# Kernel tuning notes

Hardware: AMD Instinct MI355X
Metric: run time of the kernel (lower is better)

Reference implementation:

```python
import jax, jax.numpy as jnp
import numpy as np

B, T, K = 32, 8192, 16
EPS = 1e-7
LAM_FIRE, LAM_CANCEL, LAM_VALID, LAM_WRITE = 1.0, 1.0, 0.5, 0.5


def setup_inputs() -> dict:
    key = jax.random.key(0)
    ks = jax.random.split(key, 11)
    return {
        "trigger_hazard": jax.random.uniform(ks[0], (B, T, K), jnp.float32),
        "validity": jax.random.uniform(ks[1], (B, T, K), jnp.float32),
        "cancel_logits": jax.random.normal(ks[2], (B, T, K, 3), jnp.float32),
        "write_score": jax.random.normal(ks[3], (B, T, 1), jnp.float32),
        "live_mask": jax.random.randint(ks[4], (B, T, K), 0, 2).astype(bool),
        "contract_id": jax.random.randint(ks[5], (B, T, K), 0, 32),
        "oracle_fire": jax.random.randint(ks[6], (B, T, K), 0, 2).astype(jnp.float32),
        "oracle_cancel": jax.random.randint(ks[7], (B, T, K), 0, 4),
        "oracle_valid": jax.random.randint(ks[8], (B, T, K), 0, 2).astype(jnp.float32),
        "oracle_should_write": jax.random.randint(ks[9], (B, T, 1), 0, 2).astype(jnp.float32),
        "oracle_contract_id": jax.random.randint(ks[10], (B, T, K), 0, 32),
    }


def _masked_bce(p_raw, y, m):
    # Mirrors torch: BCE(clamp(p)*mask, y*mask), then *mask, sum / clamp(mask.sum(),1)
    n = jnp.maximum(m.sum(), 1.0)
    p = jnp.clip(p_raw, EPS, 1.0 - EPS) * m
    t = y * m
    # extra inner clip only guards masked entries (p==0), which are zeroed anyway
    bce = -(t * jnp.log(jnp.clip(p, EPS)) + (1.0 - t) * jnp.log(jnp.clip(1.0 - p, EPS)))
    return (bce * m).sum() / n


def _cancel_ce(logits, cancel_tgt, live_mask):
    has = ((cancel_tgt > 0) & live_mask).astype(jnp.float32)  # (B,T,K)
    n = has.sum()
    tgt = jnp.clip(cancel_tgt - 1, 0).astype(jnp.int32)
    logp = jax.nn.log_softmax(logits, axis=-1)  # (B,T,K,3)
    ce = -jnp.take_along_axis(logp, tgt[..., None], axis=-1)[..., 0]
    return jnp.where(n > 0, (ce * has).sum() / jnp.maximum(n, 1.0), 0.0)


def _bce_with_logits(x, y):
    return jnp.mean(jnp.maximum(x, 0.0) - x * y + jnp.log1p(jnp.exp(-jnp.abs(x))))


def reference(trigger_hazard, validity, cancel_logits, write_score, live_mask,
              contract_id, oracle_fire, oracle_cancel, oracle_valid,
              oracle_should_write, oracle_contract_id):
    # Vectorized align_oracle_to_model: broadcast compare + first-match argmax + gather
    match = (contract_id[..., :, None] == oracle_contract_id[..., None, :]) \
            & (contract_id != 0)[..., None]              # (B,T,Km,Ko)
    found = match.any(axis=-1)                           # (B,T,Km)
    idx = jnp.argmax(match, axis=-1)                     # first matching oracle slot

    def align_f(x):  # float tensors -> zeros where unmatched (torch out = zeros float)
        return jnp.where(found, jnp.take_along_axis(x, idx, axis=2), 0.0)

    fire_t = align_f(oracle_fire)
    valid_t = align_f(oracle_valid)
    cancel_t = jnp.where(found, jnp.take_along_axis(oracle_cancel, idx, axis=2), 0)

    m = live_mask.astype(jnp.float32)
    fire = LAM_FIRE * _masked_bce(trigger_hazard, fire_t, m)
    cancel = LAM_CANCEL * _cancel_ce(cancel_logits, cancel_t, live_mask)
    valid = LAM_VALID * _masked_bce(validity, valid_t, m)
    write = LAM_WRITE * _bce_with_logits(write_score, oracle_should_write)
    total = fire + cancel + valid + write
    return jnp.stack([fire, cancel, valid, write, total])
```

## Files before the change

### kernel.cpp

```cpp
#include <hip/hip_runtime.h>
#include <math.h>

#define EPS_F 1e-7f

constexpr int Bc = 32, Tc = 8192, Kc = 16;
constexpr int ROWS  = Bc * Tc;
constexpr int BLOCK = 256;
constexpr int ROWS_PER_BLK = BLOCK / 4;
constexpr int NBLK  = ROWS / ROWS_PER_BLK;

typedef unsigned long long u64;

__device__ __forceinline__ u64 shflx64(u64 v, int m) {
  unsigned lo = __shfl_xor((unsigned)v, m, 64);
  unsigned hi = __shfl_xor((unsigned)(v >> 32), m, 64);
  return ((u64)hi << 32) | lo;
}

__global__ __launch_bounds__(BLOCK) void loss_main(
    const float* __restrict__ trig,
    const float* __restrict__ valp,
    const float* __restrict__ clog,
    const float* __restrict__ wscore,
    const int*   __restrict__ live,
    const int*   __restrict__ cid,
    const float* __restrict__ ofire,
    const int*   __restrict__ ocan,
    const float* __restrict__ ovalid,
    const float* __restrict__ oshw,
    const int*   __restrict__ ocid,
    float* __restrict__ part)
{
  const int t    = blockIdx.x * BLOCK + threadIdx.x;
  const int lane = threadIdx.x & 63;

  const int4   oc = ((const int4*)  ocid)[t];
  const int4   cc = ((const int4*)  ocan)[t];
  const float4 ff = ((const float4*)ofire)[t];
  const float4 vv = ((const float4*)ovalid)[t];
  const int4   cd = ((const int4*)  cid)[t];
  const int4   lm = ((const int4*)  live)[t];
  const float4 ph = ((const float4*)trig)[t];
  const float4 pq = ((const float4*)valp)[t];
  const float4 lA = ((const float4*)clog)[t * 3 + 0];
  const float4 lB = ((const float4*)clog)[t * 3 + 1];
  const float4 lC = ((const float4*)clog)[t * 3 + 2];
  float ws_x = 0.f, ws_y = 0.f;
  if (threadIdx.x < ROWS_PER_BLK) {
    const int r2 = blockIdx.x * ROWS_PER_BLK + threadIdx.x;
    ws_x = wscore[r2];
    ws_y = oshw[r2];
  }

  u64 tblLo = 0ull, tblHi = 0ull, fndLo = 0ull, fndHi = 0ull;
  {
    const int   ocs[4] = {oc.x, oc.y, oc.z, oc.w};
    const int   ccs[4] = {cc.x, cc.y, cc.z, cc.w};
    const float ffs[4] = {ff.x, ff.y, ff.z, ff.w};
    const float vvs[4] = {vv.x, vv.y, vv.z, vv.w};
    #pragma unroll
    for (int j = 0; j < 4; ++j) {
      const unsigned c  = (unsigned)ocs[j] & 31u;
      const unsigned sh = (c & 15u) * 4u;
      const bool isLo   = c < 16u;
      const u64 fsel    = isLo ? fndLo : fndHi;
      const bool seen   = ((fsel >> sh) & 1ull) != 0ull;
      const unsigned nib = (unsigned)ffs[j] | ((unsigned)vvs[j] << 1) |
                           ((unsigned)ccs[j] << 2);
      const u64 add  = seen ? 0ull : ((u64)nib << sh);
      const u64 fadd = 0xFull << sh;
      tblLo |= isLo ? add : 0ull;
      tblHi |= isLo ? 0ull : add;
      fndLo |= isLo ? fadd : 0ull;
      fndHi |= isLo ? 0ull : fadd;
    }
  }

  #pragma unroll
  for (int m = 1; m <= 2; m <<= 1) {
    const u64 pTL = shflx64(tblLo, m);
    const u64 pTH = shflx64(tblHi, m);
    const u64 pFL = shflx64(fndLo, m);
    const u64 pFH = shflx64(fndHi, m);
    const bool iLow = (lane & m) == 0;
    const u64 loTL = iLow ? tblLo : pTL, hiTL = iLow ? pTL : tblLo;
    const u64 loTH = iLow ? tblHi : pTH, hiTH = iLow ? pTH : tblHi;
    const u64 loFL = iLow ? fndLo : pFL, hiFL = iLow ? pFL : fndLo;
    const u64 loFH = iLow ? fndHi : pFH, hiFH = iLow ? pFH : fndHi;
    tblLo = loTL | (hiTL & ~loFL);
    tblHi = loTH | (hiTH & ~loFH);
    fndLo = loFL | hiFL;
    fndHi = loFH | hiFH;
  }

  float s0 = 0.f, s1 = 0.f, s2 = 0.f, s3 = 0.f, s4 = 0.f;
  {
    const int   cds[4] = {cd.x, cd.y, cd.z, cd.w};
    const int   lms[4] = {lm.x, lm.y, lm.z, lm.w};
    const float phs[4] = {ph.x, ph.y, ph.z, ph.w};
    const float pqs[4] = {pq.x, pq.y, pq.z, pq.w};
    const float L0[4] = {lA.x, lA.w, lB.z, lC.y};
    const float L1[4] = {lA.y, lB.x, lB.w, lC.z};
    const float L2[4] = {lA.z, lB.y, lC.x, lC.w};
    #pragma unroll
    for (int j = 0; j < 4; ++j) {
      const unsigned c  = (unsigned)cds[j] & 31u;
      const unsigned sh = (c & 15u) * 4u;
      const bool isLo   = c < 16u;
      const bool fnd = (c != 0u) &&
                       ((((isLo ? fndLo : fndHi) >> sh) & 1ull) != 0ull);
      unsigned nib = (unsigned)(((isLo ? tblLo : tblHi) >> sh)) & 15u;
      nib = fnd ? nib : 0u;
      const float fire_t = (float)(nib & 1u);
      const float val_t  = (float)((nib >> 1) & 1u);
      const int   can_t  = (int)(nib >> 2);

      const float m = lms[j] ? 1.f : 0.f;

      const float p  = fminf(fmaxf(phs[j], EPS_F), 1.f - EPS_F);
      const float bf = -__logf((fire_t != 0.f) ? p : 1.f - p);
      const float q  = fminf(fmaxf(pqs[j], EPS_F), 1.f - EPS_F);
      const float bv = -__logf((val_t != 0.f) ? q : 1.f - q);

      const float has = (can_t > 0 && lms[j]) ? 1.f : 0.f;
      const int tgt = (can_t - 1) < 0 ? 0 : (can_t - 1);
      const float l0 = L0[j], l1 = L1[j], l2 = L2[j];
      const float mx  = fmaxf(l0, fmaxf(l1, l2));
      const float lse = mx + __logf(__expf(l0 - mx) + __expf(l1 - mx) +
                                    __expf(l2 - mx));
      const float lt  = (tgt == 0) ? l0 : ((tgt == 1) ? l1 : l2);

      s0 += bf * m;
      s1 += m;
      s2 += (lse - lt) * has;
      s3 += has;
      s4 += bv * m;
    }
  }

  float s5 = 0.f;
  if (threadIdx.x < ROWS_PER_BLK) {
    s5 = fmaxf(ws_x, 0.f) - ws_x * ws_y + __logf(1.f + __expf(-fabsf(ws_x)));
  }

  float v[6] = {s0, s1, s2, s3, s4, s5};
  #pragma unroll
  for (int off = 32; off > 0; off >>= 1) {
    #pragma unroll
    for (int i = 0; i < 6; ++i) v[i] += __shfl_down(v[i], off, 64);
  }
  __shared__ float red[4][6];
  const int w = threadIdx.x >> 6;
  if (lane == 0) {
    #pragma unroll
    for (int i = 0; i < 6; ++i) red[w][i] = v[i];
  }
  __syncthreads();
  if (threadIdx.x == 0) {
    #pragma unroll
    for (int i = 0; i < 6; ++i)
      part[blockIdx.x * 6 + i] = red[0][i] + red[1][i] + red[2][i] + red[3][i];
  }
}

__global__ __launch_bounds__(BLOCK) void loss_finalize(
    const float* __restrict__ part, float* __restrict__ out)
{
  double v[6] = {0, 0, 0, 0, 0, 0};
  for (int r = threadIdx.x; r < NBLK; r += BLOCK) {
    #pragma unroll
    for (int i = 0; i < 6; ++i) v[i] += (double)part[r * 6 + i];
  }
  #pragma unroll
  for (int off = 32; off > 0; off >>= 1) {
    #pragma unroll
    for (int i = 0; i < 6; ++i) v[i] += __shfl_down(v[i], off, 64);
  }
  __shared__ double red[4][6];
  const int w = threadIdx.x >> 6, lane = threadIdx.x & 63;
  if (lane == 0) {
    #pragma unroll
    for (int i = 0; i < 6; ++i) red[w][i] = v[i];
  }
  __syncthreads();
  if (threadIdx.x == 0) {
    double a[6];
    #pragma unroll
    for (int i = 0; i < 6; ++i) a[i] = red[0][i] + red[1][i] + red[2][i] + red[3][i];
    const double live_n = a[1] < 1.0 ? 1.0 : a[1];
    const double fire   = a[0] / live_n;
    const double cancel = (a[3] > 0.0) ? a[2] / (a[3] < 1.0 ? 1.0 : a[3])
                                       : 0.0;
    const double valid  = 0.5 * a[4] / live_n;
    const double wr     = 0.5 * a[5] / (double)ROWS;
    out[0] = (float)fire;
    out[1] = (float)cancel;
    out[2] = (float)valid;
    out[3] = (float)wr;
    out[4] = (float)(fire + cancel + valid + wr);
  }
}

extern "C" void kernel_launch(void* const* d_in, const int* in_sizes, int n_in,
                              void* d_out, int out_size, void* d_ws, size_t ws_size,
                              hipStream_t stream) {
  const float* trig   = (const float*)d_in[0];
  const float* valp   = (const float*)d_in[1];
  const float* clog   = (const float*)d_in[2];
  const float* wscore = (const float*)d_in[3];
  const int*   live   = (const int*)  d_in[4];
  const int*   cid    = (const int*)  d_in[5];
  const float* ofire  = (const float*)d_in[6];
  const int*   ocan   = (const int*)  d_in[7];
  const float* ovalid = (const float*)d_in[8];
  const float* oshw   = (const float*)d_in[9];
  const int*   ocid   = (const int*)  d_in[10];
  float* out  = (float*)d_out;
  float* part = (float*)d_ws;

  loss_main<<<NBLK, BLOCK, 0, stream>>>(trig, valp, clog, wscore, live, cid,
                                        ofire, ocan, ovalid, oshw, ocid, part);
  loss_finalize<<<1, BLOCK, 0, stream>>>(part, out);
}
```

Before: 214.2 us.

## Use persistent-style blocks with double-buffered register prefetch of the next row group

Shrinks the grid from one row-group per thread to 1024 blocks that each loop over four strided items, prefetching the next item's loads into a second register buffer while the current one is computed. It also moves the write-score load to every fourth thread and sets a launch bound of two blocks per unit. The aim is to overlap memory latency with compute and cut the number of partial sums the finalize kernel has to reduce. In exchange, the doubled register buffers raise register pressure and lower the number of waves available to hide latency.

Result: no change. 213.1 us (-0.5%).

```diff
diff --git a/kernel.cpp b/kernel.cpp
--- a/kernel.cpp
+++ b/kernel.cpp
@@ -4,10 +4,11 @@
 #define EPS_F 1e-7f
 
 constexpr int Bc = 32, Tc = 8192, Kc = 16;
-constexpr int ROWS  = Bc * Tc;
-constexpr int BLOCK = 256;
-constexpr int ROWS_PER_BLK = BLOCK / 4;
-constexpr int NBLK  = ROWS / ROWS_PER_BLK;
+constexpr int ROWS   = Bc * Tc;
+constexpr int BLOCK  = 256;
+constexpr int NBLK   = 1024;
+constexpr int ITEMS  = 4;
+constexpr int STRIDE = NBLK * BLOCK;
 
 typedef unsigned long long u64;
 
@@ -17,7 +18,13 @@
   return ((u64)hi << 32) | lo;
 }
 
-__global__ __launch_bounds__(BLOCK) void loss_main(
+struct Item {
+  int4   oc, cc, cd, lm;
+  float4 ff, vv, ph, pq, lA, lB, lC;
+  float  wx, wy;
+};
+
+__global__ __launch_bounds__(BLOCK, 2) void loss_main(
     const float* __restrict__ trig,
     const float* __restrict__ valp,
     const float* __restrict__ clog,
@@ -31,116 +38,133 @@
     const int*   __restrict__ ocid,
     float* __restrict__ part)
 {
-  const int t    = blockIdx.x * BLOCK + threadIdx.x;
-  const int lane = threadIdx.x & 63;
-
-  const int4   oc = ((const int4*)  ocid)[t];
-  const int4   cc = ((const int4*)  ocan)[t];
-  const float4 ff = ((const float4*)ofire)[t];
-  const float4 vv = ((const float4*)ovalid)[t];
-  const int4   cd = ((const int4*)  cid)[t];
-  const int4   lm = ((const int4*)  live)[t];
-  const float4 ph = ((const float4*)trig)[t];
-  const float4 pq = ((const float4*)valp)[t];
-  const float4 lA = ((const float4*)clog)[t * 3 + 0];
-  const float4 lB = ((const float4*)clog)[t * 3 + 1];
-  const float4 lC = ((const float4*)clog)[t * 3 + 2];
-  float ws_x = 0.f, ws_y = 0.f;
-  if (threadIdx.x < ROWS_PER_BLK) {
-    const int r2 = blockIdx.x * ROWS_PER_BLK + threadIdx.x;
-    ws_x = wscore[r2];
-    ws_y = oshw[r2];
-  }
-
-  u64 tblLo = 0ull, tblHi = 0ull, fndLo = 0ull, fndHi = 0ull;
-  {
-    const int   ocs[4] = {oc.x, oc.y, oc.z, oc.w};
-    const int   ccs[4] = {cc.x, cc.y, cc.z, cc.w};
-    const float ffs[4] = {ff.x, ff.y, ff.z, ff.w};
-    const float vvs[4] = {vv.x, vv.y, vv.z, vv.w};
-    #pragma unroll
-    for (int j = 0; j < 4; ++j) {
-      const unsigned c  = (unsigned)ocs[j] & 31u;
-      const unsigned sh = (c & 15u) * 4u;
-      const bool isLo   = c < 16u;
-      const u64 fsel    = isLo ? fndLo : fndHi;
-      const bool seen   = ((fsel >> sh) & 1ull) != 0ull;
-      const unsigned nib = (unsigned)ffs[j] | ((unsigned)vvs[j] << 1) |
-                           ((unsigned)ccs[j] << 2);
-      const u64 add  = seen ? 0ull : ((u64)nib << sh);
-      const u64 fadd = 0xFull << sh;
-      tblLo |= isLo ? add : 0ull;
-      tblHi |= isLo ? 0ull : add;
-      fndLo |= isLo ? fadd : 0ull;
-      fndHi |= isLo ? 0ull : fadd;
-    }
-  }
-
+  const int  lane      = threadIdx.x & 63;
+  const bool isRowLead = (threadIdx.x & 3) == 0;
+
+  const int4*   ocid4 = (const int4*)  ocid;
+  const int4*   ocan4 = (const int4*)  ocan;
+  const float4* ofr4  = (const float4*)ofire;
+  const float4* ovl4  = (const float4*)ovalid;
+  const int4*   cid4  = (const int4*)  cid;
+  const int4*   liv4  = (const int4*)  live;
+  const float4* trg4  = (const float4*)trig;
+  const float4* vlp4  = (const float4*)valp;
+  const float4* clg4  = (const float4*)clog;
+
+  float s0 = 0.f, s1 = 0.f, s2 = 0.f, s3 = 0.f, s4 = 0.f, s5 = 0.f;
+
+  auto load_item = [&](int t, Item& it) {
+    it.oc = ocid4[t];
+    it.cc = ocan4[t];
+    it.ff = ofr4[t];
+    it.vv = ovl4[t];
+    it.cd = cid4[t];
+    it.lm = liv4[t];
+    it.ph = trg4[t];
+    it.pq = vlp4[t];
+    it.lA = clg4[t * 3 + 0];
+    it.lB = clg4[t * 3 + 1];
+    it.lC = clg4[t * 3 + 2];
+    it.wx = 0.f; it.wy = 0.f;
+    if (isRowLead) { it.wx = wscore[t >> 2]; it.wy = oshw[t >> 2]; }
+  };
+
+  auto compute = [&](const Item& it) {
+    u64 tblLo = 0ull, tblHi = 0ull, fndLo = 0ull, fndHi = 0ull;
+    {
+      const int   ocs[4] = {it.oc.x, it.oc.y, it.oc.z, it.oc.w};
+      const int   ccs[4] = {it.cc.x, it.cc.y, it.cc.z, it.cc.w};
+      const float ffs[4] = {it.ff.x, it.ff.y, it.ff.z, it.ff.w};
+      const float vvs[4] = {it.vv.x, it.vv.y, it.vv.z, it.vv.w};
+      #pragma unroll
+      for (int j = 0; j < 4; ++j) {
+        const unsigned c  = (unsigned)ocs[j] & 31u;
+        const unsigned sh = (c & 15u) * 4u;
+        const bool isLo   = c < 16u;
+        const bool seen   = (((isLo ? fndLo : fndHi) >> sh) & 1ull) != 0ull;
+        const unsigned nib = (unsigned)ffs[j] | ((unsigned)vvs[j] << 1) |
+                             ((unsigned)ccs[j] << 2);
+        const u64 add  = seen ? 0ull : ((u64)nib << sh);
+        const u64 fadd = 0xFull << sh;
+        tblLo |= isLo ? add : 0ull;
+        tblHi |= isLo ? 0ull : add;
+        fndLo |= isLo ? fadd : 0ull;
+        fndHi |= isLo ? 0ull : fadd;
+      }
+    }
+    #pragma unroll
+    for (int m = 1; m <= 2; m <<= 1) {
+      const u64 pTL = shflx64(tblLo, m);
+      const u64 pTH = shflx64(tblHi, m);
+      const u64 pFL = shflx64(fndLo, m);
+      const u64 pFH = shflx64(fndHi, m);
+      const bool iLow = (lane & m) == 0;
+      const u64 loTL = iLow ? tblLo : pTL, hiTL = iLow ? pTL : tblLo;
+      const u64 loTH = iLow ? tblHi : pTH, hiTH = iLow ? pTH : tblHi;
+      const u64 loFL = iLow ? fndLo : pFL, hiFL = iLow ? pFL : fndLo;
+      const u64 loFH = iLow ? fndHi : pFH, hiFH = iLow ? pFH : fndHi;
+      tblLo = loTL | (hiTL & ~loFL);
+      tblHi = loTH | (hiTH & ~loFH);
+      fndLo = loFL | hiFL;
+      fndHi = loFH | hiFH;
+    }
+    {
+      const int   cds[4] = {it.cd.x, it.cd.y, it.cd.z, it.cd.w};
+      const int   lms[4] = {it.lm.x, it.lm.y, it.lm.z, it.lm.w};
+      const float phs[4] = {it.ph.x, it.ph.y, it.ph.z, it.ph.w};
+      const float pqs[4] = {it.pq.x, it.pq.y, it.pq.z, it.pq.w};
+      const float L0[4] = {it.lA.x, it.lA.w, it.lB.z, it.lC.y};
+      const float L1[4] = {it.lA.y, it.lB.x, it.lB.w, it.lC.z};
+      const float L2[4] = {it.lA.z, it.lB.y, it.lC.x, it.lC.w};
+      #pragma unroll
+      for (int j = 0; j < 4; ++j) {
+        const unsigned c  = (unsigned)cds[j] & 31u;
+        const unsigned sh = (c & 15u) * 4u;
+        const bool isLo   = c < 16u;
+        const bool fnd = (c != 0u) &&
+                         ((((isLo ? fndLo : fndHi) >> sh) & 1ull) != 0ull);
+        unsigned nib = (unsigned)(((isLo ? tblLo : tblHi) >> sh)) & 15u;
+        nib = fnd ? nib : 0u;
+        const float fire_t = (float)(nib & 1u);
+        const float val_t  = (float)((nib >> 1) & 1u);
+        const int   can_t  = (int)(nib >> 2);
+
+        const float m = lms[j] ? 1.f : 0.f;
+
+        const float p  = fminf(fmaxf(phs[j], EPS_F), 1.f - EPS_F);
+        const float bf = -__logf((fire_t != 0.f) ? p : 1.f - p);
+        const float q  = fminf(fmaxf(pqs[j], EPS_F), 1.f - EPS_F);
+        const float bv = -__logf((val_t != 0.f) ? q : 1.f - q);
+
+        const float has = (can_t > 0 && lms[j]) ? 1.f : 0.f;
+        const int tgt = (can_t - 1) < 0 ? 0 : (can_t - 1);
+        const float l0 = L0[j], l1 = L1[j], l2 = L2[j];
+        const float mx  = fmaxf(l0, fmaxf(l1, l2));
+        const float lse = mx + __logf(__expf(l0 - mx) + __expf(l1 - mx) +
+                                      __expf(l2 - mx));
+        const float lt  = (tgt == 0) ? l0 : ((tgt == 1) ? l1 : l2);
+
+        s0 += bf * m;
+        s1 += m;
+        s2 += (lse - lt) * has;
+        s3 += has;
+        s4 += bv * m;
+      }
+    }
+    if (isRowLead) {
+      const float x = it.wx, y = it.wy;
+      s5 += fmaxf(x, 0.f) - x * y + __logf(1.f + __expf(-fabsf(x)));
+    }
+  };
+
+  int t = blockIdx.x * BLOCK + threadIdx.x;
+  Item buf[2];
+  load_item(t, buf[0]);
   #pragma unroll
-  for (int m = 1; m <= 2; m <<= 1) {
-    const u64 pTL = shflx64(tblLo, m);
-    const u64 pTH = shflx64(tblHi, m);
-    const u64 pFL = shflx64(fndLo, m);
-    const u64 pFH = shflx64(fndHi, m);
-    const bool iLow = (lane & m) == 0;
-    const u64 loTL = iLow ? tblLo : pTL, hiTL = iLow ? pTL : tblLo;
-    const u64 loTH = iLow ? tblHi : pTH, hiTH = iLow ? pTH : tblHi;
-    const u64 loFL = iLow ? fndLo : pFL, hiFL = iLow ? pFL : fndLo;
-    const u64 loFH = iLow ? fndHi : pFH, hiFH = iLow ? pFH : fndHi;
-    tblLo = loTL | (hiTL & ~loFL);
-    tblHi = loTH | (hiTH & ~loFH);
-    fndLo = loFL | hiFL;
-    fndHi = loFH | hiFH;
-  }
-
-  float s0 = 0.f, s1 = 0.f, s2 = 0.f, s3 = 0.f, s4 = 0.f;
-  {
-    const int   cds[4] = {cd.x, cd.y, cd.z, cd.w};
-    const int   lms[4] = {lm.x, lm.y, lm.z, lm.w};
-    const float phs[4] = {ph.x, ph.y, ph.z, ph.w};
-    const float pqs[4] = {pq.x, pq.y, pq.z, pq.w};
-    const float L0[4] = {lA.x, lA.w, lB.z, lC.y};
-    const float L1[4] = {lA.y, lB.x, lB.w, lC.z};
-    const float L2[4] = {lA.z, lB.y, lC.x, lC.w};
-    #pragma unroll
-    for (int j = 0; j < 4; ++j) {
-      const unsigned c  = (unsigned)cds[j] & 31u;
-      const unsigned sh = (c & 15u) * 4u;
-      const bool isLo   = c < 16u;
-      const bool fnd = (c != 0u) &&
-                       ((((isLo ? fndLo : fndHi) >> sh) & 1ull) != 0ull);
-      unsigned nib = (unsigned)(((isLo ? tblLo : tblHi) >> sh)) & 15u;
-      nib = fnd ? nib : 0u;
-      const float fire_t = (float)(nib & 1u);
-      const float val_t  = (float)((nib >> 1) & 1u);
-      const int   can_t  = (int)(nib >> 2);
-
-      const float m = lms[j] ? 1.f : 0.f;
-
-      const float p  = fminf(fmaxf(phs[j], EPS_F), 1.f - EPS_F);
-      const float bf = -__logf((fire_t != 0.f) ? p : 1.f - p);
-      const float q  = fminf(fmaxf(pqs[j], EPS_F), 1.f - EPS_F);
-      const float bv = -__logf((val_t != 0.f) ? q : 1.f - q);
-
-      const float has = (can_t > 0 && lms[j]) ? 1.f : 0.f;
-      const int tgt = (can_t - 1) < 0 ? 0 : (can_t - 1);
-      const float l0 = L0[j], l1 = L1[j], l2 = L2[j];
-      const float mx  = fmaxf(l0, fmaxf(l1, l2));
-      const float lse = mx + __logf(__expf(l0 - mx) + __expf(l1 - mx) +
-                                    __expf(l2 - mx));
-      const float lt  = (tgt == 0) ? l0 : ((tgt == 1) ? l1 : l2);
-
-      s0 += bf * m;
-      s1 += m;
-      s2 += (lse - lt) * has;
-      s3 += has;
-      s4 += bv * m;
-    }
-  }
-
-  float s5 = 0.f;
-  if (threadIdx.x < ROWS_PER_BLK) {
-    s5 = fmaxf(ws_x, 0.f) - ws_x * ws_y + __logf(1.f + __expf(-fabsf(ws_x)));
+  for (int i = 0; i < ITEMS; ++i) {
+    if (i + 1 < ITEMS) load_item(t + STRIDE, buf[(i + 1) & 1]);
+    compute(buf[i & 1]);
+    t += STRIDE;
   }
 
   float v[6] = {s0, s1, s2, s3, s4, s5};
```
